# Kernel tuning notes

Measured on AMD Instinct MI355X. Metric: run time of the kernel, lower is better.

Reference implementation:

```python
import jax, jax.numpy as jnp
import numpy as np

B, T, E, H, V = 64, 256, 300, 512, 50000
G = 3 * H  # gates: r, z, n (PyTorch order)


def setup_inputs() -> dict:
    key = jax.random.key(0)
    ks = jax.random.split(key, 14)
    k = 1.0 / np.sqrt(H)
    u = lambda kk, sh: jax.random.uniform(kk, sh, jnp.float32, -k, k)
    x = jax.random.randint(ks[0], (B, T), 0, V)
    emb = jax.random.normal(ks[1], (V, E), jnp.float32) * 0.1
    emb = emb.at[0].set(0.0)  # padding_idx=0
    return {
        "x": x,
        "emb": emb,
        # layer 0: input E, both directions stacked on axis 0
        "w_ih0": u(ks[2], (2, G, E)),
        "w_hh0": u(ks[3], (2, G, H)),
        "b_ih0": u(ks[4], (2, G)),
        "b_hh0": u(ks[5], (2, G)),
        # layer 1: input 2H
        "w_ih1": u(ks[6], (2, G, 2 * H)),
        "w_hh1": u(ks[7], (2, G, 2 * H if False else H)) if False else u(ks[7], (2, G, H)),
        "b_ih1": u(ks[8], (2, G)),
        "b_hh1": u(ks[9], (2, G)),
        # classifier
        "w1": u(ks[10], (128, 2 * H)),
        "b1": u(ks[11], (128,)),
        "w2": u(ks[12], (2, 128)),
        "b2": u(ks[13], (2,)),
    }


def _gru_dir(x, w_ih, w_hh, b_ih, b_hh, reverse):
    # x: [B, T, in]; precompute input projections for all timesteps
    xp = jnp.einsum('bti,gi->btg', x, w_ih) + b_ih  # [B, T, 3H]

    def step(h, xp_t):
        gh = h @ w_hh.T + b_hh  # [B, 3H]
        r = jax.nn.sigmoid(xp_t[:, :H] + gh[:, :H])
        z = jax.nn.sigmoid(xp_t[:, H:2 * H] + gh[:, H:2 * H])
        n = jnp.tanh(xp_t[:, 2 * H:] + r * gh[:, 2 * H:])
        h = (1.0 - z) * n + z * h
        return h, h

    h0 = jnp.zeros((x.shape[0], H), x.dtype)
    _, ys = jax.lax.scan(step, h0, jnp.swapaxes(xp, 0, 1), reverse=reverse)
    return jnp.swapaxes(ys, 0, 1)  # [B, T, H], aligned to input positions


def _bigru_layer(x, w_ih, w_hh, b_ih, b_hh):
    f = _gru_dir(x, w_ih[0], w_hh[0], b_ih[0], b_hh[0], False)
    b = _gru_dir(x, w_ih[1], w_hh[1], b_ih[1], b_hh[1], True)
    return jnp.concatenate([f, b], axis=-1)  # [B, T, 2H]


def reference(x, emb, w_ih0, w_hh0, b_ih0, b_hh0, w_ih1, w_hh1, b_ih1, b_hh1, w1, b1, w2, b2):
    e = emb[x]  # [B, T, E]
    h = _bigru_layer(e, w_ih0, w_hh0, b_ih0, b_hh0)
    h = _bigru_layer(h, w_ih1, w_hh1, b_ih1, b_hh1)  # dropout=eval mode (identity)
    pooled = jnp.max(h, axis=1)  # [B, 2H]
    hid = jax.nn.relu(pooled @ w1.T + b1)
    return hid @ w2.T + b2  # [B, 2]
```

## Files before the change

kernel.cpp:

```cpp
#include <hip/hip_runtime.h>

#define BB 64
#define TLEN 256
#define HH 512
#define GG 1536
#define EPAD 320
#define NN 3072
#define MM 16384

typedef __attribute__((ext_vector_type(8))) __fp16 half8;
typedef __attribute__((ext_vector_type(4))) __fp16 half4;
typedef __attribute__((ext_vector_type(4))) float floatx4;

typedef union { unsigned long long u[2]; half8 v; } hpack;
typedef union { half4 h4; unsigned long long u; } hpack4;

__global__ __launch_bounds__(256) void g2_prep(const int* __restrict__ x,
                                               const float* __restrict__ emb,
                                               __fp16* __restrict__ e,
                                               const float* __restrict__ w_ih0,
                                               __fp16* __restrict__ w0p,
                                               const float* __restrict__ w_ih1,
                                               __fp16* __restrict__ w1c) {
  const int blk = blockIdx.x;
  if (blk < 960) {
    int idx = blk * 256 + threadIdx.x;
    int row = idx / 80;
    int c = idx - row * 80;
    half4 v = {0, 0, 0, 0};
    if (c < 75) {
      float4 f = *(const float4*)&w_ih0[(long)row * 300 + c * 4];
      v[0] = (__fp16)f.x; v[1] = (__fp16)f.y; v[2] = (__fp16)f.z; v[3] = (__fp16)f.w;
    }
    *(half4*)&w0p[row * EPAD + c * 4] = v;
  } else if (blk < 2496) {
    long idx = (long)(blk - 960) * 256 + threadIdx.x;
    float4 a = *(const float4*)&w_ih1[idx * 8];
    float4 b = *(const float4*)&w_ih1[idx * 8 + 4];
    half8 o;
    o[0] = (__fp16)a.x; o[1] = (__fp16)a.y; o[2] = (__fp16)a.z; o[3] = (__fp16)a.w;
    o[4] = (__fp16)b.x; o[5] = (__fp16)b.y; o[6] = (__fp16)b.z; o[7] = (__fp16)b.w;
    *(half8*)&w1c[idx * 8] = o;
  } else {
    int idx = (blk - 2496) * 256 + threadIdx.x;
    int row = idx / 80;
    int c = idx - row * 80;
    int t = row >> 6, b = row & 63;
    half4 v = {0, 0, 0, 0};
    if (c < 75) {
      int xi = x[b * TLEN + t];
      float4 f = *(const float4*)&emb[(long)xi * 300 + c * 4];
      v[0] = (__fp16)f.x; v[1] = (__fp16)f.y; v[2] = (__fp16)f.z; v[3] = (__fp16)f.w;
    }
    *(half4*)&e[row * EPAD + c * 4] = v;
  }
}

__global__ __launch_bounds__(256) void g2_gemm(const __fp16* __restrict__ A,
                                               const __fp16* __restrict__ W,
                                               const float* __restrict__ bias,
                                               __fp16* __restrict__ C,
                                               int M, int N, int Kp) {
  __shared__ __fp16 As[128][72];
  __shared__ __fp16 Ws[128][72];
  const int nTiles = N >> 7;
  const int m0 = (blockIdx.x / nTiles) << 7;
  const int n0 = (blockIdx.x % nTiles) << 7;
  const int tid = threadIdx.x;
  const int lane = tid & 63, wv = tid >> 6;
  const int wm = (wv >> 1) << 6, wn = (wv & 1) << 6;
  const int nsub = lane & 15, quad = lane >> 4;

  floatx4 acc[4][4];
#pragma unroll
  for (int i = 0; i < 4; i++)
#pragma unroll
    for (int j = 0; j < 4; j++) acc[i][j] = (floatx4){0.f, 0.f, 0.f, 0.f};

  const int lr = tid >> 3;
  const int lc = (tid & 7) << 3;
  for (int ko = 0; ko < Kp; ko += 64) {
#pragma unroll
    for (int p = 0; p < 4; p++) {
      int r = lr + p * 32;
      *(half8*)&As[r][lc] = *(const half8*)&A[(long)(m0 + r) * Kp + ko + lc];
      *(half8*)&Ws[r][lc] = *(const half8*)&W[(long)(n0 + r) * Kp + ko + lc];
    }
    __syncthreads();
#pragma unroll
    for (int kk = 0; kk < 64; kk += 32) {
      half8 af[4], bf[4];
      const int kr = kk + (quad << 3);
#pragma unroll
      for (int i = 0; i < 4; i++) af[i] = *(const half8*)&As[wm + i * 16 + nsub][kr];
#pragma unroll
      for (int j = 0; j < 4; j++) bf[j] = *(const half8*)&Ws[wn + j * 16 + nsub][kr];
#pragma unroll
      for (int i = 0; i < 4; i++)
#pragma unroll
        for (int j = 0; j < 4; j++)
          acc[i][j] = __builtin_amdgcn_mfma_f32_16x16x32_f16(af[i], bf[j], acc[i][j], 0, 0, 0);
    }
    __syncthreads();
  }
#pragma unroll
  for (int j = 0; j < 4; j++) {
    int col = n0 + wn + j * 16 + nsub;
    float bv = bias[col];
#pragma unroll
    for (int i = 0; i < 4; i++) {
      int rb = m0 + wm + i * 16 + (quad << 2);
#pragma unroll
      for (int ii = 0; ii < 4; ii++)
        C[(long)(rb + ii) * N + col] = (__fp16)(acc[i][j][ii] + bv);
    }
  }
}

__global__ __launch_bounds__(256, 1) void g2_rnn(const float* __restrict__ whh,
                                                 const float* __restrict__ bhh,
                                                 const __fp16* __restrict__ xp,
                                                 __fp16* __restrict__ hout,
                                                 __fp16* __restrict__ hx) {
  __shared__ __fp16 Wl[96][520];
  const unsigned long long SENT = 0xFFFFFFFFFFFFFFFFULL;
  const int bid = blockIdx.x;
  const int gi = bid & 3;
  const int uo = bid >> 2;
  const int d = gi >> 1, g = gi & 1;
  const int tid = threadIdx.x;
  const int lane = tid & 63, wv = tid >> 6;
  const int U0 = uo << 5;
  const int mb = wv & 1, ut = wv >> 1;
  const int nsub = lane & 15, quad = lane >> 4;
  const int bq = (g << 5) + (mb << 4);
  const int ul = (ut << 4) + nsub;

  const float* wd = whh + (long)d * (GG * HH);
  for (int idx = tid; idx < 96 * 64; idx += 256) {
    int r = idx >> 6;
    int c = (idx & 63) << 3;
    int gate = r >> 5, u2 = r & 31;
    const float* src = &wd[(long)(gate * HH + U0 + u2) * HH + c];
    float4 a = *(const float4*)&src[0];
    float4 b = *(const float4*)&src[4];
    half8 o;
    o[0] = (__fp16)a.x; o[1] = (__fp16)a.y; o[2] = (__fp16)a.z; o[3] = (__fp16)a.w;
    o[4] = (__fp16)b.x; o[5] = (__fp16)b.y; o[6] = (__fp16)b.z; o[7] = (__fp16)b.w;
    *(half8*)&Wl[r][c] = o;
  }
  __syncthreads();

  half8 wr_[16], wz_[16], wn_[16];
#pragma unroll
  for (int kk = 0; kk < 16; kk++) {
    const int kcol = (kk << 5) + (quad << 3);
    wr_[kk] = *(const half8*)&Wl[ul][kcol];
    wz_[kk] = *(const half8*)&Wl[32 + ul][kcol];
    wn_[kk] = *(const half8*)&Wl[64 + ul][kcol];
  }

  const int ub = (ut << 4) + (quad << 2);
  const float* bb = bhh + d * GG + U0 + ub;
  float4 bhr4 = *(const float4*)&bb[0];
  float4 bhz4 = *(const float4*)&bb[HH];
  float4 bhn4 = *(const float4*)&bb[2 * HH];

  const int cidx = ((quad >> 1) << 6) + (nsub << 2) + ((quad & 1) << 1);
  const int pidx = (uo << 7) + (ut << 6) + (nsub << 2) + quad;

  float hprev[4] = {0.f, 0.f, 0.f, 0.f};

  for (int s = 0; s < TLEN; s++) {
    const int tt = d ? (TLEN - 1 - s) : s;
    half4 xr4, xz4, xn4;
    {
      const __fp16* xb = xp + (long)(tt * BB + bq + nsub) * NN + d * GG + U0 + ub;
      xr4 = *(const half4*)&xb[0];
      xz4 = *(const half4*)&xb[HH];
      xn4 = *(const half4*)&xb[2 * HH];
    }
    floatx4 ar0 = {0.f, 0.f, 0.f, 0.f}, ar1 = ar0, az0 = ar0, az1 = ar0, an0 = ar0, an1 = ar0;
    if (s > 0) {
      const int pt = d ? (tt + 1) : (tt - 1);
      const unsigned long long* hx8 =
          (const unsigned long long*)(hx + ((((long)pt * 2 + d) * 2 + g) * 2 + mb) * 8192);
      hpack u[16];
      int bad;
      do {
#pragma unroll
        for (int kk = 0; kk < 16; kk++) {
          u[kk].u[0] = __hip_atomic_load(&hx8[kk * 128 + cidx], __ATOMIC_RELAXED, __HIP_MEMORY_SCOPE_AGENT);
          u[kk].u[1] = __hip_atomic_load(&hx8[kk * 128 + cidx + 1], __ATOMIC_RELAXED, __HIP_MEMORY_SCOPE_AGENT);
        }
        bad = 0;
#pragma unroll
        for (int kk = 0; kk < 16; kk++)
          bad |= (u[kk].u[0] == SENT) | (u[kk].u[1] == SENT);
      } while (__any(bad));
#pragma unroll
      for (int kk = 0; kk < 16; kk += 2) {
        ar0 = __builtin_amdgcn_mfma_f32_16x16x32_f16(wr_[kk], u[kk].v, ar0, 0, 0, 0);
        az0 = __builtin_amdgcn_mfma_f32_16x16x32_f16(wz_[kk], u[kk].v, az0, 0, 0, 0);
        an0 = __builtin_amdgcn_mfma_f32_16x16x32_f16(wn_[kk], u[kk].v, an0, 0, 0, 0);
        ar1 = __builtin_amdgcn_mfma_f32_16x16x32_f16(wr_[kk + 1], u[kk + 1].v, ar1, 0, 0, 0);
        az1 = __builtin_amdgcn_mfma_f32_16x16x32_f16(wz_[kk + 1], u[kk + 1].v, az1, 0, 0, 0);
        an1 = __builtin_amdgcn_mfma_f32_16x16x32_f16(wn_[kk + 1], u[kk + 1].v, an1, 0, 0, 0);
      }
    }
    hpack4 pk;
#pragma unroll
    for (int i = 0; i < 4; i++) {
      float grv = ar0[i] + ar1[i] + (float)xr4[i] + bhr4[i];
      float gzv = az0[i] + az1[i] + (float)xz4[i] + bhz4[i];
      float gnv = an0[i] + an1[i] + bhn4[i];
      float rg = 1.f / (1.f + __expf(-grv));
      float zg = 1.f / (1.f + __expf(-gzv));
      float ex = __expf(2.f * ((float)xn4[i] + rg * gnv));
      float ng = 1.f - 2.f / (ex + 1.f);
      float hv = (1.f - zg) * ng + zg * hprev[i];
      hprev[i] = hv;
      pk.h4[i] = (__fp16)hv;
    }
    {
      unsigned long long* hxw =
          (unsigned long long*)(hx + ((((long)tt * 2 + d) * 2 + g) * 2 + mb) * 8192);
      __hip_atomic_store(&hxw[pidx], pk.u, __ATOMIC_RELAXED, __HIP_MEMORY_SCOPE_AGENT);
      *(half4*)&hout[(long)(tt * BB + bq + nsub) * 1024 + d * HH + U0 + ub] = pk.h4;
    }
  }
}

__global__ __launch_bounds__(256) void g2_pool(const __fp16* __restrict__ h1,
                                               float* __restrict__ pooled) {
  int b = blockIdx.x;
  int j0 = threadIdx.x * 4;
  float m[4] = {-3e38f, -3e38f, -3e38f, -3e38f};
  const __fp16* p = h1 + b * 1024 + j0;
  for (int t = 0; t < TLEN; t++) {
    half4 v = *(const half4*)(p + (long)t * BB * 1024);
#pragma unroll
    for (int q = 0; q < 4; q++) m[q] = fmaxf(m[q], (float)v[q]);
  }
  float* o = pooled + b * 1024 + j0;
#pragma unroll
  for (int q = 0; q < 4; q++) o[q] = m[q];
}

__global__ __launch_bounds__(128) void g2_head(const float* __restrict__ pooled,
                                               const float* __restrict__ w1,
                                               const float* __restrict__ b1,
                                               const float* __restrict__ w2,
                                               const float* __restrict__ b2,
                                               float* __restrict__ out) {
  __shared__ float pl[1024];
  __shared__ float hid[128];
  int b = blockIdx.x, j = threadIdx.x;
  for (int k = j; k < 1024; k += 128) pl[k] = pooled[b * 1024 + k];
  __syncthreads();
  float acc = b1[j];
  const float* wr = w1 + (long)j * 1024;
  for (int k = 0; k < 1024; k += 4) {
    float4 w = *(const float4*)&wr[k];
    acc += pl[k] * w.x + pl[k + 1] * w.y + pl[k + 2] * w.z + pl[k + 3] * w.w;
  }
  hid[j] = fmaxf(acc, 0.f);
  __syncthreads();
  if (j < 2) {
    float a = b2[j];
    for (int k = 0; k < 128; k++) a += hid[k] * w2[j * 128 + k];
    out[b * 2 + j] = a;
  }
}

extern "C" void kernel_launch(void* const* d_in, const int* in_sizes, int n_in,
                              void* d_out, int out_size, void* d_ws, size_t ws_size,
                              hipStream_t stream) {
  (void)in_sizes; (void)n_in; (void)out_size; (void)ws_size;
  const int* x = (const int*)d_in[0];
  const float* emb = (const float*)d_in[1];
  const float* w_ih0 = (const float*)d_in[2];
  const float* w_hh0 = (const float*)d_in[3];
  const float* b_ih0 = (const float*)d_in[4];
  const float* b_hh0 = (const float*)d_in[5];
  const float* w_ih1 = (const float*)d_in[6];
  const float* w_hh1 = (const float*)d_in[7];
  const float* b_ih1 = (const float*)d_in[8];
  const float* b_hh1 = (const float*)d_in[9];
  const float* w1 = (const float*)d_in[10];
  const float* b1 = (const float*)d_in[11];
  const float* w2 = (const float*)d_in[12];
  const float* b2 = (const float*)d_in[13];

  char* ws = (char*)d_ws;
  __fp16* xp = (__fp16*)(ws + 0);
  __fp16* h0 = (__fp16*)(ws + 100663296);
  __fp16* h1 = (__fp16*)(ws + 134217728);
  __fp16* e_pad = (__fp16*)(ws + 167772160);
  __fp16* w0p = (__fp16*)(ws + 178257920);
  __fp16* w1c = (__fp16*)(ws + 180224000);
  float* pooled = (float*)(ws + 186515456);

  (void)hipMemsetAsync(h1, 0xFF, 33554432, stream);
  g2_prep<<<7616, 256, 0, stream>>>(x, emb, e_pad, w_ih0, w0p, w_ih1, w1c);
  g2_gemm<<<3072, 256, 0, stream>>>(e_pad, w0p, b_ih0, xp, MM, NN, EPAD);
  g2_rnn<<<64, 256, 0, stream>>>(w_hh0, b_hh0, xp, h0, h1);
  g2_gemm<<<3072, 256, 0, stream>>>(h0, w1c, b_ih1, xp, MM, NN, 1024);
  (void)hipMemsetAsync(h0, 0xFF, 33554432, stream);
  g2_rnn<<<64, 256, 0, stream>>>(w_hh1, b_hh1, xp, h1, h0);
  g2_pool<<<64, 256, 0, stream>>>(h1, pooled);
  g2_head<<<64, 128, 0, stream>>>(pooled, w1, b1, w2, b2, (float*)d_out);
}
```

Before: 2.109 ms.

## Merge batch halves into one RNN block to overlap h-exchange latency

Each recurrent block now handles both 32-row batch halves instead of one, halving the grid from 64 to 32 blocks. Both halves' previous hidden states are loaded up front, so one half's exchange latency can overlap with the other half's MFMA and gate math. This also halves the number of blocks in the cross-block spin-wait sync. The cost is twice the serial compute per block per step, more register pressure, and fewer CUs in use.

```diff
diff --git a/kernel.cpp b/kernel.cpp
--- a/kernel.cpp
+++ b/kernel.cpp
@@ -125,15 +125,13 @@
   __shared__ __fp16 Wl[96][520];
   const unsigned long long SENT = 0xFFFFFFFFFFFFFFFFULL;
   const int bid = blockIdx.x;
-  const int gi = bid & 3;
-  const int uo = bid >> 2;
-  const int d = gi >> 1, g = gi & 1;
+  const int d = bid & 1;
+  const int uo = bid >> 1;
   const int tid = threadIdx.x;
   const int lane = tid & 63, wv = tid >> 6;
   const int U0 = uo << 5;
   const int mb = wv & 1, ut = wv >> 1;
   const int nsub = lane & 15, quad = lane >> 4;
-  const int bq = (g << 5) + (mb << 4);
   const int ul = (ut << 4) + nsub;
 
   const float* wd = whh + (long)d * (GG * HH);
@@ -169,64 +167,135 @@
   const int cidx = ((quad >> 1) << 6) + (nsub << 2) + ((quad & 1) << 1);
   const int pidx = (uo << 7) + (ut << 6) + (nsub << 2) + quad;
 
-  float hprev[4] = {0.f, 0.f, 0.f, 0.f};
+  float hprev0[4] = {0.f, 0.f, 0.f, 0.f};
+  float hprev1[4] = {0.f, 0.f, 0.f, 0.f};
 
   for (int s = 0; s < TLEN; s++) {
     const int tt = d ? (TLEN - 1 - s) : s;
-    half4 xr4, xz4, xn4;
+    half4 xr40, xz40, xn40, xr41, xz41, xn41;
     {
-      const __fp16* xb = xp + (long)(tt * BB + bq + nsub) * NN + d * GG + U0 + ub;
-      xr4 = *(const half4*)&xb[0];
-      xz4 = *(const half4*)&xb[HH];
-      xn4 = *(const half4*)&xb[2 * HH];
-    }
-    floatx4 ar0 = {0.f, 0.f, 0.f, 0.f}, ar1 = ar0, az0 = ar0, az1 = ar0, an0 = ar0, an1 = ar0;
+      const __fp16* xb0 = xp + (long)(tt * BB + (mb << 4) + nsub) * NN + d * GG + U0 + ub;
+      const __fp16* xb1 = xb0 + (long)32 * NN;
+      xr40 = *(const half4*)&xb0[0];
+      xz40 = *(const half4*)&xb0[HH];
+      xn40 = *(const half4*)&xb0[2 * HH];
+      xr41 = *(const half4*)&xb1[0];
+      xz41 = *(const half4*)&xb1[HH];
+      xn41 = *(const half4*)&xb1[2 * HH];
+    }
+    hpack u0[16], u1[16];
+    const unsigned long long* hx80 = 0;
+    const unsigned long long* hx81 = 0;
     if (s > 0) {
       const int pt = d ? (tt + 1) : (tt - 1);
-      const unsigned long long* hx8 =
-          (const unsigned long long*)(hx + ((((long)pt * 2 + d) * 2 + g) * 2 + mb) * 8192);
-      hpack u[16];
-      int bad;
-      do {
-#pragma unroll
-        for (int kk = 0; kk < 16; kk++) {
-          u[kk].u[0] = __hip_atomic_load(&hx8[kk * 128 + cidx], __ATOMIC_RELAXED, __HIP_MEMORY_SCOPE_AGENT);
-          u[kk].u[1] = __hip_atomic_load(&hx8[kk * 128 + cidx + 1], __ATOMIC_RELAXED, __HIP_MEMORY_SCOPE_AGENT);
+      hx80 = (const unsigned long long*)(hx + ((((long)pt * 2 + d) * 2 + 0) * 2 + mb) * 8192);
+      hx81 = (const unsigned long long*)(hx + ((((long)pt * 2 + d) * 2 + 1) * 2 + mb) * 8192);
+#pragma unroll
+      for (int kk = 0; kk < 16; kk++) {
+        u0[kk].u[0] = __hip_atomic_load(&hx80[kk * 128 + cidx], __ATOMIC_RELAXED, __HIP_MEMORY_SCOPE_AGENT);
+        u0[kk].u[1] = __hip_atomic_load(&hx80[kk * 128 + cidx + 1], __ATOMIC_RELAXED, __HIP_MEMORY_SCOPE_AGENT);
+      }
+#pragma unroll
+      for (int kk = 0; kk < 16; kk++) {
+        u1[kk].u[0] = __hip_atomic_load(&hx81[kk * 128 + cidx], __ATOMIC_RELAXED, __HIP_MEMORY_SCOPE_AGENT);
+        u1[kk].u[1] = __hip_atomic_load(&hx81[kk * 128 + cidx + 1], __ATOMIC_RELAXED, __HIP_MEMORY_SCOPE_AGENT);
+      }
+    }
+
+    {
+      floatx4 ar0 = {0.f, 0.f, 0.f, 0.f}, ar1 = ar0, az0 = ar0, az1 = ar0, an0 = ar0, an1 = ar0;
+      if (s > 0) {
+        int bad = 0;
+#pragma unroll
+        for (int kk = 0; kk < 16; kk++)
+          bad |= (u0[kk].u[0] == SENT) | (u0[kk].u[1] == SENT);
+        while (__any(bad)) {
+#pragma unroll
+          for (int kk = 0; kk < 16; kk++) {
+            u0[kk].u[0] = __hip_atomic_load(&hx80[kk * 128 + cidx], __ATOMIC_RELAXED, __HIP_MEMORY_SCOPE_AGENT);
+            u0[kk].u[1] = __hip_atomic_load(&hx80[kk * 128 + cidx + 1], __ATOMIC_RELAXED, __HIP_MEMORY_SCOPE_AGENT);
+          }
+          bad = 0;
+#pragma unroll
+          for (int kk = 0; kk < 16; kk++)
+            bad |= (u0[kk].u[0] == SENT) | (u0[kk].u[1] == SENT);
         }
-        bad = 0;
+#pragma unroll
+        for (int kk = 0; kk < 16; kk += 2) {
+          ar0 = __builtin_amdgcn_mfma_f32_16x16x32_f16(wr_[kk], u0[kk].v, ar0, 0, 0, 0);
+          az0 = __builtin_amdgcn_mfma_f32_16x16x32_f16(wz_[kk], u0[kk].v, az0, 0, 0, 0);
+          an0 = __builtin_amdgcn_mfma_f32_16x16x32_f16(wn_[kk], u0[kk].v, an0, 0, 0, 0);
+          ar1 = __builtin_amdgcn_mfma_f32_16x16x32_f16(wr_[kk + 1], u0[kk + 1].v, ar1, 0, 0, 0);
+          az1 = __builtin_amdgcn_mfma_f32_16x16x32_f16(wz_[kk + 1], u0[kk + 1].v, az1, 0, 0, 0);
+          an1 = __builtin_amdgcn_mfma_f32_16x16x32_f16(wn_[kk + 1], u0[kk + 1].v, an1, 0, 0, 0);
+        }
+      }
+      hpack4 pk;
+#pragma unroll
+      for (int i = 0; i < 4; i++) {
+        float grv = ar0[i] + ar1[i] + (float)xr40[i] + bhr4[i];
+        float gzv = az0[i] + az1[i] + (float)xz40[i] + bhz4[i];
+        float gnv = an0[i] + an1[i] + bhn4[i];
+        float rg = 1.f / (1.f + __expf(-grv));
+        float zg = 1.f / (1.f + __expf(-gzv));
+        float ex = __expf(2.f * ((float)xn40[i] + rg * gnv));
+        float ng = 1.f - 2.f / (ex + 1.f);
+        float hv = (1.f - zg) * ng + zg * hprev0[i];
+        hprev0[i] = hv;
+        pk.h4[i] = (__fp16)hv;
+      }
+      unsigned long long* hxw =
+          (unsigned long long*)(hx + ((((long)tt * 2 + d) * 2 + 0) * 2 + mb) * 8192);
+      __hip_atomic_store(&hxw[pidx], pk.u, __ATOMIC_RELAXED, __HIP_MEMORY_SCOPE_AGENT);
+      *(half4*)&hout[(long)(tt * BB + (mb << 4) + nsub) * 1024 + d * HH + U0 + ub] = pk.h4;
+    }
+
+    {
+      floatx4 ar0 = {0.f, 0.f, 0.f, 0.f}, ar1 = ar0, az0 = ar0, az1 = ar0, an0 = ar0, an1 = ar0;
+      if (s > 0) {
+        int bad = 0;
 #pragma unroll
         for (int kk = 0; kk < 16; kk++)
-          bad |= (u[kk].u[0] == SENT) | (u[kk].u[1] == SENT);
-      } while (__any(bad));
-#pragma unroll
-      for (int kk = 0; kk < 16; kk += 2) {
-        ar0 = __builtin_amdgcn_mfma_f32_16x16x32_f16(wr_[kk], u[kk].v, ar0, 0, 0, 0);
-        az0 = __builtin_amdgcn_mfma_f32_16x16x32_f16(wz_[kk], u[kk].v, az0, 0, 0, 0);
-        an0 = __builtin_amdgcn_mfma_f32_16x16x32_f16(wn_[kk], u[kk].v, an0, 0, 0, 0);
-        ar1 = __builtin_amdgcn_mfma_f32_16x16x32_f16(wr_[kk + 1], u[kk + 1].v, ar1, 0, 0, 0);
-        az1 = __builtin_amdgcn_mfma_f32_16x16x32_f16(wz_[kk + 1], u[kk + 1].v, az1, 0, 0, 0);
-        an1 = __builtin_amdgcn_mfma_f32_16x16x32_f16(wn_[kk + 1], u[kk + 1].v, an1, 0, 0, 0);
-      }
-    }
-    hpack4 pk;
-#pragma unroll
-    for (int i = 0; i < 4; i++) {
-      float grv = ar0[i] + ar1[i] + (float)xr4[i] + bhr4[i];
-      float gzv = az0[i] + az1[i] + (float)xz4[i] + bhz4[i];
-      float gnv = an0[i] + an1[i] + bhn4[i];
-      float rg = 1.f / (1.f + __expf(-grv));
-      float zg = 1.f / (1.f + __expf(-gzv));
-      float ex = __expf(2.f * ((float)xn4[i] + rg * gnv));
-      float ng = 1.f - 2.f / (ex + 1.f);
-      float hv = (1.f - zg) * ng + zg * hprev[i];
-      hprev[i] = hv;
-      pk.h4[i] = (__fp16)hv;
-    }
-    {
+          bad |= (u1[kk].u[0] == SENT) | (u1[kk].u[1] == SENT);
+        while (__any(bad)) {
+#pragma unroll
+          for (int kk = 0; kk < 16; kk++) {
+            u1[kk].u[0] = __hip_atomic_load(&hx81[kk * 128 + cidx], __ATOMIC_RELAXED, __HIP_MEMORY_SCOPE_AGENT);
+            u1[kk].u[1] = __hip_atomic_load(&hx81[kk * 128 + cidx + 1], __ATOMIC_RELAXED, __HIP_MEMORY_SCOPE_AGENT);
+          }
+          bad = 0;
+#pragma unroll
+          for (int kk = 0; kk < 16; kk++)
+            bad |= (u1[kk].u[0] == SENT) | (u1[kk].u[1] == SENT);
+        }
+#pragma unroll
+        for (int kk = 0; kk < 16; kk += 2) {
+          ar0 = __builtin_amdgcn_mfma_f32_16x16x32_f16(wr_[kk], u1[kk].v, ar0, 0, 0, 0);
+          az0 = __builtin_amdgcn_mfma_f32_16x16x32_f16(wz_[kk], u1[kk].v, az0, 0, 0, 0);
+          an0 = __builtin_amdgcn_mfma_f32_16x16x32_f16(wn_[kk], u1[kk].v, an0, 0, 0, 0);
+          ar1 = __builtin_amdgcn_mfma_f32_16x16x32_f16(wr_[kk + 1], u1[kk + 1].v, ar1, 0, 0, 0);
+          az1 = __builtin_amdgcn_mfma_f32_16x16x32_f16(wz_[kk + 1], u1[kk + 1].v, az1, 0, 0, 0);
+          an1 = __builtin_amdgcn_mfma_f32_16x16x32_f16(wn_[kk + 1], u1[kk + 1].v, an1, 0, 0, 0);
+        }
+      }
+      hpack4 pk;
+#pragma unroll
+      for (int i = 0; i < 4; i++) {
+        float grv = ar0[i] + ar1[i] + (float)xr41[i] + bhr4[i];
+        float gzv = az0[i] + az1[i] + (float)xz41[i] + bhz4[i];
+        float gnv = an0[i] + an1[i] + bhn4[i];
+        float rg = 1.f / (1.f + __expf(-grv));
+        float zg = 1.f / (1.f + __expf(-gzv));
+        float ex = __expf(2.f * ((float)xn41[i] + rg * gnv));
+        float ng = 1.f - 2.f / (ex + 1.f);
+        float hv = (1.f - zg) * ng + zg * hprev1[i];
+        hprev1[i] = hv;
+        pk.h4[i] = (__fp16)hv;
+      }
       unsigned long long* hxw =
-          (unsigned long long*)(hx + ((((long)tt * 2 + d) * 2 + g) * 2 + mb) * 8192);
+          (unsigned long long*)(hx + ((((long)tt * 2 + d) * 2 + 1) * 2 + mb) * 8192);
       __hip_atomic_store(&hxw[pidx], pk.u, __ATOMIC_RELAXED, __HIP_MEMORY_SCOPE_AGENT);
-      *(half4*)&hout[(long)(tt * BB + bq + nsub) * 1024 + d * HH + U0 + ub] = pk.h4;
+      *(half4*)&hout[(long)(tt * BB + 32 + (mb << 4) + nsub) * 1024 + d * HH + U0 + ub] = pk.h4;
     }
   }
 }
@@ -304,10 +373,10 @@
   (void)hipMemsetAsync(h1, 0xFF, 33554432, stream);
   g2_prep<<<7616, 256, 0, stream>>>(x, emb, e_pad, w_ih0, w0p, w_ih1, w1c);
   g2_gemm<<<3072, 256, 0, stream>>>(e_pad, w0p, b_ih0, xp, MM, NN, EPAD);
-  g2_rnn<<<64, 256, 0, stream>>>(w_hh0, b_hh0, xp, h0, h1);
+  g2_rnn<<<32, 256, 0, stream>>>(w_hh0, b_hh0, xp, h0, h1);
   g2_gemm<<<3072, 256, 0, stream>>>(h0, w1c, b_ih1, xp, MM, NN, 1024);
   (void)hipMemsetAsync(h0, 0xFF, 33554432, stream);
-  g2_rnn<<<64, 256, 0, stream>>>(w_hh1, b_hh1, xp, h1, h0);
+  g2_rnn<<<32, 256, 0, stream>>>(w_hh1, b_hh1, xp, h1, h0);
   g2_pool<<<64, 256, 0, stream>>>(h1, pooled);
   g2_head<<<64, 128, 0, stream>>>(pooled, w1, b1, w2, b2, (float*)d_out);
 }
```

Result: slower. 4.255 ms (+101.8%).
